# Kernel tuning notes

Hardware: AMD Instinct MI355X
Metric: run time of the kernel (lower is better)

The kernel has to match this reference:

```python
import jax, jax.numpy as jnp
import numpy as np

B, T, CH, V, E, L = 64, 1024, 256, 32000, 64, 128  # batch, enc_len, channel, vocab, emb_dim, latent_dims


def setup_inputs() -> dict:
    key = jax.random.key(0)
    ks = jax.random.split(key, 13)
    s = 0.05  # weight init scale
    return {
        "prev_cont_vec": jax.random.normal(ks[0], (B, CH), jnp.float32),
        "F": jax.random.normal(ks[1], (B, T, CH), jnp.float32),
        "prev_char": jax.random.normal(ks[2], (B, V), jnp.float32),
        "state_h": jax.random.normal(ks[3], (B, L), jnp.float32),
        "state_c": jax.random.normal(ks[4], (B, L), jnp.float32),
        # learned parameters (all Dense layers use_bias=False)
        "Wc": jax.random.normal(ks[5], (V, E), jnp.float32) * s,
        "Wct1": jax.random.normal(ks[6], (CH, E), jnp.float32) * s,
        "Wo": jax.random.normal(ks[7], (L, V), jnp.float32) * s,
        "Wct2": jax.random.normal(ks[8], (CH, V), jnp.float32) * s,
        "lstm_kernel": jax.random.normal(ks[9], (E, 4 * L), jnp.float32) * s,
        "lstm_recurrent": jax.random.normal(ks[10], (L, 4 * L), jnp.float32) * s,
        "W_h": jax.random.normal(ks[11], (L, CH), jnp.float32) * s,
        "V_attn": jax.random.normal(ks[12], (1, 1, CH), jnp.float32) * s,
    }


def reference(prev_cont_vec, F, prev_char, state_h, state_c,
              Wc, Wct1, Wo, Wct2, lstm_kernel, lstm_recurrent, W_h, V_attn):
    # lstm input: Wc(prev_char) + Wct1(prev_cont_vec)  -> [B, E]
    lstm_inp = prev_char @ Wc + prev_cont_vec @ Wct1
    # Keras LSTMCell (no bias), gate order i, f, c, o
    z = lstm_inp @ lstm_kernel + state_h @ lstm_recurrent  # [B, 4L]
    zi, zf, zg, zo = jnp.split(z, 4, axis=-1)
    i = jax.nn.sigmoid(zi)
    f = jax.nn.sigmoid(zf)
    g = jnp.tanh(zg)
    o = jax.nn.sigmoid(zo)
    new_c = f * state_c + i * g
    new_h = o * jnp.tanh(new_c)
    # training=True branch: clip returned cell state
    new_c_out = jnp.clip(new_c, -10.0, 10.0)
    # additive attention over time axis of F [B, T, CH]
    H_tfm = (new_h @ W_h)[:, None, :]            # [B, 1, CH]
    e_t = V_attn * jnp.tanh(H_tfm + F)           # [B, T, CH]
    attn = jax.nn.softmax(e_t, axis=1)           # softmax over T, per channel
    c_t = jnp.sum(attn * F, axis=1)              # [B, CH]
    # output distribution
    O_t = jax.nn.softmax(new_h @ Wo + c_t @ Wct2, axis=1)  # [B, V]
    return (O_t, c_t, new_h, new_c_out)
```

## Files before the change

### kernel.cpp

```cpp
#include <hip/hip_runtime.h>
#include <hip/hip_bf16.h>

#define BB 64
#define TT 1024
#define CHN 256
#define VV 32000
#define EE 64
#define LL 128
#define NC1 250
#define KC1 128
#define TS 8

typedef unsigned short u16;
typedef unsigned int u32;

__device__ __forceinline__ float fast_rcp(float x) { return __builtin_amdgcn_rcpf(x); }
__device__ __forceinline__ float tanh_fast(float y) {
    float e = __expf(2.0f * y);
    return 1.0f - 2.0f * fast_rcp(1.0f + e);
}
__device__ __forceinline__ float sigmoid_fast(float x) {
    return fast_rcp(1.0f + __expf(-x));
}

__global__ __launch_bounds__(256) void k1_stage1(const float* __restrict__ A,
                                                 const float* __restrict__ Wc,
                                                 float* __restrict__ part) {
    const int kc = blockIdx.x;
    const int k0 = kc * KC1;
    const int e  = threadIdx.x & 63;
    const int b0 = blockIdx.y * 32 + __builtin_amdgcn_readfirstlane(threadIdx.x >> 6) * 8;

    float acc[8];
    #pragma unroll
    for (int i = 0; i < 8; ++i) acc[i] = 0.0f;

    const float* W  = Wc + (size_t)k0 * EE + e;
    const float* Ar = A + (size_t)b0 * VV + k0;
    float wa[8], wb[8];
    #pragma unroll
    for (int j = 0; j < 8; ++j) wa[j] = W[(size_t)j * EE];

    for (int k = 0; k < KC1; k += 16) {
        #pragma unroll
        for (int j = 0; j < 8; ++j) wb[j] = W[(size_t)(k + 8 + j) * EE];
        #pragma unroll
        for (int j = 0; j < 8; ++j) {
            #pragma unroll
            for (int i = 0; i < 8; ++i)
                acc[i] = fmaf(Ar[(size_t)i * VV + k + j], wa[j], acc[i]);
        }
        if (k + 16 < KC1) {
            #pragma unroll
            for (int j = 0; j < 8; ++j) wa[j] = W[(size_t)(k + 16 + j) * EE];
        }
        #pragma unroll
        for (int j = 0; j < 8; ++j) {
            #pragma unroll
            for (int i = 0; i < 8; ++i)
                acc[i] = fmaf(Ar[(size_t)i * VV + k + 8 + j], wb[j], acc[i]);
        }
    }
    float* dst = part + (size_t)kc * (BB * EE) + b0 * EE + e;
    #pragma unroll
    for (int i = 0; i < 8; ++i) dst[i * EE] = acc[i];
}

__global__ __launch_bounds__(512) void k2_lstm(const float* __restrict__ part,
    const float* __restrict__ pcv, const float* __restrict__ state_h,
    const float* __restrict__ state_c, const float* __restrict__ Wct1,
    const float* __restrict__ lstm_kernel, const float* __restrict__ lstm_rec,
    const float* __restrict__ W_h,
    float* __restrict__ out_newh, float* __restrict__ out_newc,
    float* __restrict__ At, float* __restrict__ Htfm) {
    __shared__ float red[8][EE];
    __shared__ float inp[EE];
    __shared__ float sh[LL];
    __shared__ float z[4 * LL];
    __shared__ float nh[LL];
    const int b = blockIdx.x;
    const int t = threadIdx.x;
    const int e  = t & 63;
    const int g  = t >> 6;

    {
        float s = 0.0f;
        for (int j = g; j < NC1; j += 8)
            s += part[(size_t)j * (BB * EE) + b * EE + e];
        const int c0 = g * 32;
        #pragma unroll 8
        for (int c = 0; c < 32; ++c)
            s = fmaf(pcv[b * CHN + c0 + c], Wct1[(size_t)(c0 + c) * EE + e], s);
        red[g][e] = s;
    }
    __syncthreads();
    if (t < EE) {
        float s = 0.0f;
        #pragma unroll
        for (int j = 0; j < 8; ++j) s += red[j][t];
        inp[t] = s;
    } else if (t >= 64 && t < 64 + LL) {
        sh[t - 64] = state_h[b * LL + (t - 64)];
    }
    __syncthreads();
    {
        float a = 0.0f;
        #pragma unroll 8
        for (int e2 = 0; e2 < EE; ++e2) a = fmaf(inp[e2], lstm_kernel[e2 * 512 + t], a);
        #pragma unroll 8
        for (int l = 0; l < LL; ++l) a = fmaf(sh[l], lstm_rec[l * 512 + t], a);
        z[t] = a;
    }
    __syncthreads();
    if (t < LL) {
        float zi = z[t], zf = z[LL + t], zg = z[2 * LL + t], zo = z[3 * LL + t];
        float ig = sigmoid_fast(zi);
        float fg = sigmoid_fast(zf);
        float gg = tanh_fast(zg);
        float og = sigmoid_fast(zo);
        float co = state_c[b * LL + t];
        float cn = fg * co + ig * gg;
        float hn = og * tanh_fast(cn);
        out_newc[b * LL + t] = fminf(fmaxf(cn, -10.0f), 10.0f);
        out_newh[b * LL + t] = hn;
        At[t * BB + b] = hn;
        nh[t] = hn;
    }
    __syncthreads();
    if (t < CHN) {
        float a = 0.0f;
        #pragma unroll 8
        for (int l = 0; l < LL; ++l) a = fmaf(nh[l], W_h[l * CHN + t], a);
        Htfm[b * CHN + t] = a;
    }
}

__global__ __launch_bounds__(256) void k3_attn(const float* __restrict__ F,
    const float* __restrict__ Htfm, const float* __restrict__ Vattn,
    float* __restrict__ pS, float* __restrict__ pW) {
    __shared__ float4 sS[256];
    __shared__ float4 sW[256];
    const int b    = blockIdx.x;
    const int ts   = blockIdx.y;
    const int lane = threadIdx.x & 63;
    const int w    = threadIdx.x >> 6;
    const int ch   = lane * 4;

    float4 h = *(const float4*)(Htfm + b * CHN + ch);
    float4 v = *(const float4*)(Vattn + ch);
    float s0 = 0, s1 = 0, s2 = 0, s3 = 0;
    float a0 = 0, a1 = 0, a2 = 0, a3 = 0;

    const float* Fp = F + ((size_t)b * TT + ts * (TT / TS) + w * 32) * CHN + ch;
    #pragma unroll 4
    for (int t = 0; t < 32; ++t) {
        float4 f = *(const float4*)(Fp + (size_t)t * CHN);
        float e0 = __expf(v.x * tanh_fast(h.x + f.x));
        float e1 = __expf(v.y * tanh_fast(h.y + f.y));
        float e2 = __expf(v.z * tanh_fast(h.z + f.z));
        float e3 = __expf(v.w * tanh_fast(h.w + f.w));
        s0 += e0; s1 += e1; s2 += e2; s3 += e3;
        a0 = fmaf(e0, f.x, a0); a1 = fmaf(e1, f.y, a1);
        a2 = fmaf(e2, f.z, a2); a3 = fmaf(e3, f.w, a3);
    }
    sS[threadIdx.x] = make_float4(s0, s1, s2, s3);
    sW[threadIdx.x] = make_float4(a0, a1, a2, a3);
    __syncthreads();
    if (threadIdx.x < 64) {
        float4 S = sS[threadIdx.x];
        float4 W = sW[threadIdx.x];
        #pragma unroll
        for (int j = 1; j < 4; ++j) {
            float4 s = sS[j * 64 + threadIdx.x];
            float4 q = sW[j * 64 + threadIdx.x];
            S.x += s.x; S.y += s.y; S.z += s.z; S.w += s.w;
            W.x += q.x; W.y += q.y; W.z += q.z; W.w += q.w;
        }
        int base = (b * TS + ts) * CHN + threadIdx.x * 4;
        *(float4*)(pS + base) = S;
        *(float4*)(pW + base) = W;
    }
}

__global__ __launch_bounds__(256) void k4_combine(const float* __restrict__ pS,
    const float* __restrict__ pW, float* __restrict__ out_ct, float* __restrict__ At,
    float* __restrict__ rowsum) {
    const int b = blockIdx.x;
    const int ch = threadIdx.x;
    float S = 0.0f, W = 0.0f;
    #pragma unroll
    for (int j = 0; j < TS; ++j) {
        int idx = (b * TS + j) * CHN + ch;
        S += pS[idx];
        W += pW[idx];
    }
    float c = W / S;
    out_ct[b * CHN + ch] = c;
    At[(LL + ch) * BB + b] = c;
    if (b == 0 && ch < BB) rowsum[ch] = 0.0f;
}

__device__ __forceinline__ void k5_phase(const float* __restrict__ W, int kn,
    const float* __restrict__ Abase, float acc[8]) {
    float wa[8], wb[8];
    #pragma unroll
    for (int j = 0; j < 8; ++j) wa[j] = W[(size_t)j * VV];
    for (int k = 0; k < kn; k += 16) {
        #pragma unroll
        for (int j = 0; j < 8; ++j) wb[j] = W[(size_t)(k + 8 + j) * VV];
        #pragma unroll
        for (int j = 0; j < 8; ++j) {
            const float* a = Abase + (size_t)(k + j) * BB;
            #pragma unroll
            for (int i = 0; i < 8; ++i) acc[i] = fmaf(a[i], wa[j], acc[i]);
        }
        if (k + 16 < kn) {
            #pragma unroll
            for (int j = 0; j < 8; ++j) wa[j] = W[(size_t)(k + 16 + j) * VV];
        }
        #pragma unroll
        for (int j = 0; j < 8; ++j) {
            const float* a = Abase + (size_t)(k + 8 + j) * BB;
            #pragma unroll
            for (int i = 0; i < 8; ++i) acc[i] = fmaf(a[i], wb[j], acc[i]);
        }
    }
}

__global__ __launch_bounds__(256) void k5_logits(const float* __restrict__ Wo,
    const float* __restrict__ Wct2, const float* __restrict__ At,
    float* __restrict__ outO) {
    const int v  = blockIdx.x * 64 + (threadIdx.x & 63);
    const int b0 = blockIdx.y * 32 + __builtin_amdgcn_readfirstlane(threadIdx.x >> 6) * 8;
    float acc[8];
    #pragma unroll
    for (int i = 0; i < 8; ++i) acc[i] = 0.0f;

    k5_phase(Wo + v, LL, At + b0, acc);
    k5_phase(Wct2 + v, CHN, At + (size_t)LL * BB + b0, acc);

    #pragma unroll
    for (int i = 0; i < 8; ++i) outO[(size_t)(b0 + i) * VV + v] = acc[i];
}

__global__ __launch_bounds__(256) void k5b_expsum(const float* __restrict__ O,
                                                  float* __restrict__ rowsum) {
    __shared__ float red[256];
    const int b = blockIdx.x;
    const int c = blockIdx.y;
    const int t = threadIdx.x;
    const float4* row4 = (const float4*)(O + (size_t)b * VV);

    float s = 0.0f;
    for (int i = c * 2000 + t; i < (c + 1) * 2000; i += 256) {
        float4 f = row4[i];
        s += __expf(f.x) + __expf(f.y) + __expf(f.z) + __expf(f.w);
    }
    red[t] = s;
    __syncthreads();
    for (int off = 128; off > 0; off >>= 1) {
        if (t < off) red[t] += red[t + off];
        __syncthreads();
    }
    if (t == 0) atomicAdd(&rowsum[b], red[0]);
}

__global__ __launch_bounds__(256) void k5c_norm(float* __restrict__ O,
                                                const float* __restrict__ rowsum) {
    const int gid = blockIdx.x * 256 + threadIdx.x;
    float4* O4 = (float4*)O;
    const u32 row = ((u32)gid * 4u) / (u32)VV;
    const float inv = fast_rcp(rowsum[row]);
    float4 f = O4[gid];
    f.x = __expf(f.x) * inv;
    f.y = __expf(f.y) * inv;
    f.z = __expf(f.z) * inv;
    f.w = __expf(f.w) * inv;
    O4[gid] = f;
}

extern "C" void kernel_launch(void* const* d_in, const int* in_sizes, int n_in,
                              void* d_out, int out_size, void* d_ws, size_t ws_size,
                              hipStream_t stream) {
    (void)in_sizes; (void)n_in; (void)out_size; (void)ws_size;
    const float* pcv       = (const float*)d_in[0];
    const float* F         = (const float*)d_in[1];
    const float* prev_char = (const float*)d_in[2];
    const float* state_h   = (const float*)d_in[3];
    const float* state_c   = (const float*)d_in[4];
    const float* Wc        = (const float*)d_in[5];
    const float* Wct1      = (const float*)d_in[6];
    const float* Wo        = (const float*)d_in[7];
    const float* Wct2      = (const float*)d_in[8];
    const float* lstm_k    = (const float*)d_in[9];
    const float* lstm_r    = (const float*)d_in[10];
    const float* W_h       = (const float*)d_in[11];
    const float* Vattn     = (const float*)d_in[12];

    float* outO  = (float*)d_out;
    float* outCt = outO + (size_t)BB * VV;
    float* outH  = outCt + (size_t)BB * CHN;
    float* outC  = outH + (size_t)BB * LL;

    float* ws     = (float*)d_ws;
    float* part   = ws;
    float* pS     = part + (size_t)NC1 * BB * EE;
    float* pW     = pS + (size_t)BB * TS * CHN;
    float* At     = pW + (size_t)BB * TS * CHN;
    float* Htfm   = At + (LL + CHN) * BB;
    float* rowsum = part;

    hipLaunchKernelGGL(k1_stage1, dim3(NC1, 2), dim3(256), 0, stream, prev_char, Wc, part);
    hipLaunchKernelGGL(k2_lstm, dim3(BB), dim3(512), 0, stream, part, pcv, state_h,
                       state_c, Wct1, lstm_k, lstm_r, W_h, outH, outC, At, Htfm);
    hipLaunchKernelGGL(k3_attn, dim3(BB, TS), dim3(256), 0, stream, F, Htfm, Vattn, pS, pW);
    hipLaunchKernelGGL(k4_combine, dim3(BB), dim3(256), 0, stream, pS, pW, outCt, At, rowsum);
    hipLaunchKernelGGL(k5_logits, dim3(VV / 64, 2), dim3(256), 0, stream, Wo, Wct2, At, outO);
    hipLaunchKernelGGL(k5b_expsum, dim3(BB, 4), dim3(256), 0, stream, outO, rowsum);
    hipLaunchKernelGGL(k5c_norm, dim3((BB * VV / 4) / 256), dim3(256), 0, stream, outO, rowsum);
}
```

Measured before the change: 257.0 us.

## Fuse exp and row-sum into logits kernel, re-split attention and partial layout

```diff
diff --git a/kernel.cpp b/kernel.cpp
--- a/kernel.cpp
+++ b/kernel.cpp
@@ -9,7 +9,7 @@
 #define LL 128
 #define NC1 250
 #define KC1 128
-#define TS 8
+#define TS 16
 
 typedef unsigned short u16;
 typedef unsigned int u32;
@@ -61,9 +61,9 @@
                 acc[i] = fmaf(Ar[(size_t)i * VV + k + 8 + j], wb[j], acc[i]);
         }
     }
-    float* dst = part + (size_t)kc * (BB * EE) + b0 * EE + e;
-    #pragma unroll
-    for (int i = 0; i < 8; ++i) dst[i * EE] = acc[i];
+    #pragma unroll
+    for (int i = 0; i < 8; ++i)
+        part[((size_t)(b0 + i) * NC1 + kc) * EE + e] = acc[i];
 }
 
 __global__ __launch_bounds__(512) void k2_lstm(const float* __restrict__ part,
@@ -86,7 +86,7 @@
     {
         float s = 0.0f;
         for (int j = g; j < NC1; j += 8)
-            s += part[(size_t)j * (BB * EE) + b * EE + e];
+            s += part[((size_t)b * NC1 + j) * EE + e];
         const int c0 = g * 32;
         #pragma unroll 8
         for (int c = 0; c < 32; ++c)
@@ -151,17 +151,20 @@
     float s0 = 0, s1 = 0, s2 = 0, s3 = 0;
     float a0 = 0, a1 = 0, a2 = 0, a3 = 0;
 
-    const float* Fp = F + ((size_t)b * TT + ts * (TT / TS) + w * 32) * CHN + ch;
-    #pragma unroll 4
-    for (int t = 0; t < 32; ++t) {
-        float4 f = *(const float4*)(Fp + (size_t)t * CHN);
-        float e0 = __expf(v.x * tanh_fast(h.x + f.x));
-        float e1 = __expf(v.y * tanh_fast(h.y + f.y));
-        float e2 = __expf(v.z * tanh_fast(h.z + f.z));
-        float e3 = __expf(v.w * tanh_fast(h.w + f.w));
+    const float* Fp = F + ((size_t)b * TT + ts * (TT / TS) + w * 16) * CHN + ch;
+    float4 cur = *(const float4*)(Fp);
+    #pragma unroll
+    for (int t = 0; t < 16; ++t) {
+        float4 nxt;
+        if (t < 15) nxt = *(const float4*)(Fp + (size_t)(t + 1) * CHN);
+        float e0 = __expf(v.x * tanh_fast(h.x + cur.x));
+        float e1 = __expf(v.y * tanh_fast(h.y + cur.y));
+        float e2 = __expf(v.z * tanh_fast(h.z + cur.z));
+        float e3 = __expf(v.w * tanh_fast(h.w + cur.w));
         s0 += e0; s1 += e1; s2 += e2; s3 += e3;
-        a0 = fmaf(e0, f.x, a0); a1 = fmaf(e1, f.y, a1);
-        a2 = fmaf(e2, f.z, a2); a3 = fmaf(e3, f.w, a3);
+        a0 = fmaf(e0, cur.x, a0); a1 = fmaf(e1, cur.y, a1);
+        a2 = fmaf(e2, cur.z, a2); a3 = fmaf(e3, cur.w, a3);
+        cur = nxt;
     }
     sS[threadIdx.x] = make_float4(s0, s1, s2, s3);
     sW[threadIdx.x] = make_float4(a0, a1, a2, a3);
@@ -227,11 +230,12 @@
     }
 }
 
-__global__ __launch_bounds__(256) void k5_logits(const float* __restrict__ Wo,
+__global__ __launch_bounds__(512) void k5_logits(const float* __restrict__ Wo,
     const float* __restrict__ Wct2, const float* __restrict__ At,
-    float* __restrict__ outO) {
-    const int v  = blockIdx.x * 64 + (threadIdx.x & 63);
-    const int b0 = blockIdx.y * 32 + __builtin_amdgcn_readfirstlane(threadIdx.x >> 6) * 8;
+    float* __restrict__ outO, float* __restrict__ rowsum) {
+    const int lane = threadIdx.x & 63;
+    const int v  = blockIdx.x * 64 + lane;
+    const int b0 = __builtin_amdgcn_readfirstlane(threadIdx.x >> 6) * 8;
     float acc[8];
     #pragma unroll
     for (int i = 0; i < 8; ++i) acc[i] = 0.0f;
@@ -239,30 +243,23 @@
     k5_phase(Wo + v, LL, At + b0, acc);
     k5_phase(Wct2 + v, CHN, At + (size_t)LL * BB + b0, acc);
 
-    #pragma unroll
-    for (int i = 0; i < 8; ++i) outO[(size_t)(b0 + i) * VV + v] = acc[i];
-}
-
-__global__ __launch_bounds__(256) void k5b_expsum(const float* __restrict__ O,
-                                                  float* __restrict__ rowsum) {
-    __shared__ float red[256];
-    const int b = blockIdx.x;
-    const int c = blockIdx.y;
-    const int t = threadIdx.x;
-    const float4* row4 = (const float4*)(O + (size_t)b * VV);
-
-    float s = 0.0f;
-    for (int i = c * 2000 + t; i < (c + 1) * 2000; i += 256) {
-        float4 f = row4[i];
-        s += __expf(f.x) + __expf(f.y) + __expf(f.z) + __expf(f.w);
-    }
-    red[t] = s;
-    __syncthreads();
-    for (int off = 128; off > 0; off >>= 1) {
-        if (t < off) red[t] += red[t + off];
-        __syncthreads();
-    }
-    if (t == 0) atomicAdd(&rowsum[b], red[0]);
+    float ex[8];
+    #pragma unroll
+    for (int i = 0; i < 8; ++i) {
+        ex[i] = __expf(acc[i]);
+        outO[(size_t)(b0 + i) * VV + v] = ex[i];
+    }
+    #pragma unroll
+    for (int i = 0; i < 8; ++i) {
+        float s = ex[i];
+        #pragma unroll
+        for (int m = 32; m > 0; m >>= 1) s += __shfl_xor(s, m);
+        ex[i] = s;
+    }
+    if (lane == 0) {
+        #pragma unroll
+        for (int i = 0; i < 8; ++i) atomicAdd(&rowsum[b0 + i], ex[i]);
+    }
 }
 
 __global__ __launch_bounds__(256) void k5c_norm(float* __restrict__ O,
@@ -272,10 +269,7 @@
     const u32 row = ((u32)gid * 4u) / (u32)VV;
     const float inv = fast_rcp(rowsum[row]);
     float4 f = O4[gid];
-    f.x = __expf(f.x) * inv;
-    f.y = __expf(f.y) * inv;
-    f.z = __expf(f.z) * inv;
-    f.w = __expf(f.w) * inv;
+    f.x *= inv; f.y *= inv; f.z *= inv; f.w *= inv;
     O4[gid] = f;
 }
 
@@ -315,7 +309,6 @@
                        state_c, Wct1, lstm_k, lstm_r, W_h, outH, outC, At, Htfm);
     hipLaunchKernelGGL(k3_attn, dim3(BB, TS), dim3(256), 0, stream, F, Htfm, Vattn, pS, pW);
     hipLaunchKernelGGL(k4_combine, dim3(BB), dim3(256), 0, stream, pS, pW, outCt, At, rowsum);
-    hipLaunchKernelGGL(k5_logits, dim3(VV / 64, 2), dim3(256), 0, stream, Wo, Wct2, At, outO);
-    hipLaunchKernelGGL(k5b_expsum, dim3(BB, 4), dim3(256), 0, stream, outO, rowsum);
+    hipLaunchKernelGGL(k5_logits, dim3(VV / 64), dim3(512), 0, stream, Wo, Wct2, At, outO, rowsum);
     hipLaunchKernelGGL(k5c_norm, dim3((BB * VV / 4) / 256), dim3(256), 0, stream, outO, rowsum);
 }
```

New measurement: 443.1 us. +72.4%, slower.
